# Optimization experiments

Measured on AMD Instinct MI355X. Metric: run time of the kernel, lower is better.

## Reference

```python
import jax, jax.numpy as jnp
import numpy as np

B = 32
N = 1024  # half_size == num_delays == num_wavelength
DELTA_TAU = 1.5e-15
W_CENTER = 1.175e15  # center_frequency / 2
PULSE_THRESHOLD = 0.01
PENALTY = 10.0
REAL_W = 1.0; IMAG_W = 1.0; INT_W = 1.0; PHASE_W = 1.0; FROG_W = 1.0
MSE_WSUM = REAL_W + IMAG_W + INT_W + PHASE_W

# Hilbert mask exactly as in the torch source (even N branch): H[N//2+1:]=2, H[N//2]=1
_Hm = np.zeros(N, dtype=np.float32)
_Hm[N // 2 + 1:] = 2.0
_Hm[N // 2] = 1.0
HILBERT_MASK = jnp.asarray(_Hm)

# precomputed circular-shift gather indices: shifted[m, j] = x[(j - delay[m]) mod N]
_delays = np.arange(-(N // 2), N // 2)
SHIFT_IDX = jnp.asarray((np.arange(N)[None, :] - _delays[:, None]) % N)  # [N, N] int
SHIFT_FACTOR = jnp.exp(-1j * jnp.asarray(2.0 * W_CENTER * DELTA_TAU * _delays, dtype=jnp.float32)).astype(jnp.complex64)  # [N]


def hilbert(x):  # x: [N] real -> [N] complex analytical signal
    xf = jnp.fft.fft(x)
    return jnp.fft.ifft(xf * HILBERT_MASK)


def shg_mat(a):  # a: [N] complex -> [N, N] complex SHG matrix (vectorized createSHGmat)
    shifted = a[SHIFT_IDX]                                  # [N, N] all circular shifts
    rows = a[None, :] * shifted * SHIFT_FACTOR[None, :]     # elementwise complex multiply
    f = jnp.fft.fft(jnp.fft.fftshift(rows, axes=-1), axis=-1)  # one batched FFT
    return DELTA_TAU * jnp.fft.fftshift(f, axes=-1)


def _first_last(mask):  # mask: [B, N] bool -> per-sample first/last significant index with fallback
    any_m = jnp.any(mask, axis=1)
    first = jnp.where(any_m, jnp.argmax(mask, axis=1), 0)
    last = jnp.where(any_m, N - 1 - jnp.argmax(mask[:, ::-1], axis=1), N - 1)
    return first, last


def setup_inputs() -> dict:
    key = jax.random.key(0)
    k1, k2, k3 = jax.random.split(key, 3)
    prediction = jax.random.normal(k1, (B, N), dtype=jnp.float32)
    label = jax.random.normal(k2, (B, 2 * N), dtype=jnp.float32)
    shg_matrix = jax.random.uniform(k3, (B, 1, N, N), dtype=jnp.float32)
    return {"prediction": prediction, "label": label, "shg_matrix": shg_matrix}


def reference(prediction, label, shg_matrix):
    pa = jax.vmap(hilbert)(prediction)          # [B, N] complex64
    pr, pi = pa.real, pa.imag
    lr, li = label[:, :N], label[:, N:]
    l_int = lr ** 2 + li ** 2
    p_int = pr ** 2 + pi ** 2
    l_ph = jnp.arctan2(li, lr)
    p_ph = jnp.arctan2(pi, pr)

    # ---- FROG error ----
    shg_pred = jnp.abs(jax.vmap(shg_mat)(pa)) ** 2              # [B, N, N]
    shg_pred = shg_pred / jnp.max(shg_pred, axis=(1, 2), keepdims=True)  # normalizeSHGmatrix
    t_ref = shg_matrix[:, 0]                                    # [B, N, N]
    sum1 = jnp.sum(shg_pred * t_ref, axis=(1, 2))
    sum2 = jnp.sum(t_ref * t_ref, axis=(1, 2))
    mu = sum1 / sum2
    r = jnp.sum(shg_pred - mu[:, None, None] * t_ref, axis=(1, 2)) ** 2
    norm = (N * N) * jnp.max(shg_pred, axis=(1, 2)) ** 2
    frog = jnp.where(r == 0.0, 0.0, jnp.sqrt(r / norm))         # [B]

    # ---- weighted masked MSE ----
    fr, lr_idx = _first_last(jnp.abs(lr) > PULSE_THRESHOLD)
    fi, li_idx = _first_last(jnp.abs(li) > PULSE_THRESHOLD)
    first = jnp.minimum(fr, fi)
    last = jnp.maximum(lr_idx, li_idx)
    ar = jnp.arange(N)[None, :]
    in_range = (ar >= first[:, None]) & (ar < last[:, None])    # [first:last] slice semantics
    phase_mask = in_range.astype(jnp.float32)
    pulse_mask = jnp.where(in_range, PENALTY, 1.0)

    mse_real = jnp.mean((pr - lr) ** 2 * pulse_mask, axis=1) * REAL_W
    mse_imag = jnp.mean((pi - li) ** 2 * pulse_mask, axis=1) * IMAG_W
    mse_int = jnp.mean((p_int - l_int) ** 2 * pulse_mask, axis=1) * INT_W
    mse_ph = jnp.mean((p_ph - l_ph) ** 2 * phase_mask, axis=1) * PHASE_W
    mse = (mse_real + mse_imag + mse_int + mse_ph) / MSE_WSUM

    return jnp.mean(mse + FROG_W * frog)
```

## Files before the change

### kernel.cpp

```cpp
#include <hip/hip_runtime.h>
#include <math.h>

#define N 1024
#define BATCH 32
#define NT 256
#define ROWS 4

#define WSYNC() asm volatile("s_waitcnt lgkmcnt(0)" ::: "memory")

typedef float2 cf;
__device__ __forceinline__ cf cadd(cf a, cf b){ return make_float2(a.x+b.x, a.y+b.y); }
__device__ __forceinline__ cf csub(cf a, cf b){ return make_float2(a.x-b.x, a.y-b.y); }
__device__ __forceinline__ cf cmul(cf a, cf b){ return make_float2(a.x*b.x - a.y*b.y, a.x*b.y + a.y*b.x); }

__device__ __forceinline__ cf twiddle(float jn){
    float s = __builtin_amdgcn_sinf(jn);
    float c = __builtin_amdgcn_cosf(jn);
    return make_float2(c, -s);
}

__device__ __forceinline__ void bfly(cf x0, cf x1, cf x2, cf x3,
                                     cf& y0, cf& y1, cf& y2, cf& y3){
    cf A = cadd(x0,x2), Bs = cadd(x1,x3);
    cf C = csub(x0,x2), D = csub(x1,x3);
    cf Dmi = make_float2(D.y, -D.x);
    y0 = cadd(A,Bs); y1 = cadd(C,Dmi); y2 = csub(A,Bs); y3 = csub(C,Dmi);
}

__global__ __launch_bounds__(64) void hconv_k(const float* __restrict__ pred,
                                              const float* __restrict__ label,
                                              cf* __restrict__ a,
                                              cf* __restrict__ ca,
                                              float* __restrict__ mseP) {
    __shared__ float xe[512], xo[512], C2[1024];
    int l = threadIdx.x, blk = blockIdx.x;
    int b = blk >> 3, oct = blk & 7;
    const float* xr = pred + b * N;

    float4 q0 = *(const float4*)(xr + 16 * l);
    float4 q1 = *(const float4*)(xr + 16 * l + 4);
    float4 q2 = *(const float4*)(xr + 16 * l + 8);
    float4 q3 = *(const float4*)(xr + 16 * l + 12);
    *(float4*)&xe[8 * l]     = make_float4(q0.x, q0.z, q1.x, q1.z);
    *(float4*)&xe[8 * l + 4] = make_float4(q2.x, q2.z, q3.x, q3.z);
    *(float4*)&xo[8 * l]     = make_float4(q0.y, q0.w, q1.y, q1.w);
    *(float4*)&xo[8 * l + 4] = make_float4(q2.y, q2.w, q3.y, q3.w);
    float lsum = q0.x+q0.y+q0.z+q0.w + q1.x+q1.y+q1.z+q1.w
               + q2.x+q2.y+q2.z+q2.w + q3.x+q3.y+q3.z+q3.w;
    for (int o = 32; o > 0; o >>= 1) lsum += __shfl_down(lsum, o);
    float mean = __shfl(lsum, 0) * (1.f / 1024.f);

#pragma unroll
    for (int k = 0; k < 16; ++k) {
        int u = l + 64 * k;
        int j = u & 511;
        float th = (float)(2 * j + 1) * (3.14159274f / 1024.f);
        C2[u] = -(cosf(th) / sinf(th)) * (1.f / 512.f);
    }
    WSYNC();

    int v = oct * 64 + l;
    int P = v + 512;
    float acc_e = 0.f, acc_o = 0.f;
    float c_hi = C2[P];
    for (int c = 0; c < 128; ++c) {
        float4 xep = *(const float4*)&xe[4 * c];
        float4 xop = *(const float4*)&xo[4 * c];
        float c0 = C2[P - 1 - 4 * c];
        float c1 = C2[P - 2 - 4 * c];
        float c2 = C2[P - 3 - 4 * c];
        float c3 = C2[P - 4 - 4 * c];
        acc_e += xop.x * c0;  acc_o += xep.x * c_hi;
        acc_e += xop.y * c1;  acc_o += xep.y * c0;
        acc_e += xop.z * c2;  acc_o += xep.z * c1;
        acc_e += xop.w * c3;  acc_o += xep.w * c2;
        c_hi = c3;
    }

    int ne = 2 * v, no = ne + 1;
    float axe = xe[v] - mean, axo = xo[v] - mean;
    *(float4*)&a[b * N + ne] = make_float4(axe, acc_e, axo, acc_o);
    float pe = (float)(3.525 * (double)(ne - 512));
    float po = (float)(3.525 * (double)(no - 512));
    float se, cE, so_, cO;
    sincosf(pe, &se, &cE);
    sincosf(po, &so_, &cO);
    *(float4*)&ca[b * N + ne] = make_float4(axe * cE + acc_e * se, acc_e * cE - axe * se,
                                            axo * cO + acc_o * so_, acc_o * cO - axo * so_);

    const float* lab = label + b * 2 * N;
    int mnR = N, mxR = -1, mnI = N, mxI = -1;
#pragma unroll
    for (int k = 0; k < 16; ++k) {
        int n = l + 64 * k;
        float lr = lab[n], li = lab[N + n];
        if (fabsf(lr) > 0.01f) { mnR = min(mnR, n); mxR = max(mxR, n); }
        if (fabsf(li) > 0.01f) { mnI = min(mnI, n); mxI = max(mxI, n); }
    }
    for (int o = 32; o > 0; o >>= 1) {
        mnR = min(mnR, __shfl_down(mnR, o));
        mxR = max(mxR, __shfl_down(mxR, o));
        mnI = min(mnI, __shfl_down(mnI, o));
        mxI = max(mxI, __shfl_down(mxI, o));
    }
    mnR = __shfl(mnR, 0); mxR = __shfl(mxR, 0);
    mnI = __shfl(mnI, 0); mxI = __shfl(mxI, 0);
    int fr   = (mnR == N) ? 0 : mnR;
    int lstR = (mxR < 0) ? (N - 1) : mxR;
    int fi   = (mnI == N) ? 0 : mnI;
    int lstI = (mxI < 0) ? (N - 1) : mxI;
    int first = min(fr, fi), last = max(lstR, lstI);

    float s_lane = 0.f;
    {
        float lr = lab[ne], li = lab[N + ne];
        bool in = (ne >= first) && (ne < last);
        float pm = in ? 10.f : 1.f, phm = in ? 1.f : 0.f;
        float dr = axe - lr, di = acc_e - li;
        float dn = (axe * axe + acc_e * acc_e) - (lr * lr + li * li);
        float dp = atan2f(acc_e, axe) - atan2f(li, lr);
        s_lane += (dr * dr + di * di + dn * dn) * pm + dp * dp * phm;

        lr = lab[no]; li = lab[N + no];
        in = (no >= first) && (no < last);
        pm = in ? 10.f : 1.f; phm = in ? 1.f : 0.f;
        dr = axo - lr; di = acc_o - li;
        dn = (axo * axo + acc_o * acc_o) - (lr * lr + li * li);
        dp = atan2f(acc_o, axo) - atan2f(li, lr);
        s_lane += (dr * dr + di * di + dn * dn) * pm + dp * dp * phm;
    }
    for (int o = 32; o > 0; o >>= 1) s_lane += __shfl_down(s_lane, o);
    if (l == 0) mseP[blk] = s_lane;
}

__global__ __launch_bounds__(NT) void shg_k(const cf* __restrict__ a,
                                            const cf* __restrict__ cag,
                                            const float* __restrict__ tref,
                                            float* __restrict__ Praw,
                                            float* __restrict__ Prt,
                                            float* __restrict__ Pmax,
                                            float* __restrict__ Pt,
                                            float* __restrict__ Ptt) {
    __shared__ cf wk[ROWS * N];
    int t = threadIdx.x, blk = blockIdx.x;
    int b = blk >> 8;
    int dg = (blk & 255) << 2;
    const cf* arow  = a   + b * N;
    const cf* carow = cag + b * N;

    int r3 = t >> 6;
    int g  = t & 63;
    int bd = b * N + dg + r3;
    int kb = ((g & 3) << 4) | (g & 12) | (g >> 4);
    const float* trow2 = tref + ((size_t)bd << 10) + kb;
    float tv[16];
#pragma unroll
    for (int u = 0; u < 4; ++u)
#pragma unroll
        for (int m = 0; m < 4; ++m)
            tv[4*u + m] = trow2[(((m + 2) & 3) << 8) | (u << 6)];

    {
        int bt = t;
        cf w1 = twiddle((float)bt * (1.0f / 1024.0f));
        cf w2 = cmul(w1,w1), w3 = cmul(w2,w1);
        cf cv[4];
#pragma unroll
        for (int j = 0; j < 4; ++j) cv[j] = carow[bt + 256*j];
        int wb = bt ^ (((bt >> 4) & 7) << 1);
#pragma unroll
        for (int r = 0; r < ROWS; ++r) {
            int d = dg + r;
            cf x[4];
#pragma unroll
            for (int k = 0; k < 4; ++k)
                x[k] = cmul(cv[(k + 2) & 3], arow[(bt + 256*k - d) & 1023]);
            cf y0, y1, y2, y3; bfly(x[0],x[1],x[2],x[3],y0,y1,y2,y3);
            cf* w = wk + r * N + wb;
            w[0]   = y0;
            w[256] = cmul(y1,w1);
            w[512] = cmul(y2,w2);
            w[768] = cmul(y3,w3);
        }
    }
    __syncthreads();

    __builtin_amdgcn_s_setprio(1);
    {
        int r  = t >> 6;
        int q2 = t & 63;
        int B2 = q2 >> 4;
        int v  = q2 & 15;
        cf* w = wk + r * N + B2 * 256;
        cf p[16];
#pragma unroll
        for (int m = 0; m < 16; ++m) p[m] = w[16*m + (v ^ ((m & 7) << 1))];
        {
            const cf T16 = { 0.923879533f, -0.382683432f };
            cf w1 = twiddle((float)v * (1.0f / 256.0f));
#pragma unroll
            for (int m0 = 0; m0 < 4; ++m0) {
                cf w2 = cmul(w1,w1), w3 = cmul(w2,w1);
                cf y0, y1, y2, y3;
                bfly(p[m0], p[m0+4], p[m0+8], p[m0+12], y0,y1,y2,y3);
                p[m0]    = y0;
                p[m0+4]  = cmul(y1,w1);
                p[m0+8]  = cmul(y2,w2);
                p[m0+12] = cmul(y3,w3);
                w1 = cmul(w1, T16);
            }
        }
        {
            cf w1 = twiddle((float)v * (1.0f / 64.0f));
            cf w2 = cmul(w1,w1), w3 = cmul(w2,w1);
#pragma unroll
            for (int s = 0; s < 4; ++s) {
                cf y0, y1, y2, y3;
                bfly(p[4*s], p[4*s+1], p[4*s+2], p[4*s+3], y0,y1,y2,y3);
                p[4*s]   = y0;
                p[4*s+1] = cmul(y1,w1);
                p[4*s+2] = cmul(y2,w2);
                p[4*s+3] = cmul(y3,w3);
            }
        }
#pragma unroll
        for (int m = 0; m < 16; ++m) w[16*m + (v ^ ((m & 7) << 1))] = p[m];
    }
    WSYNC();

    {
        const cf W1 = { 0.923879533f, -0.382683432f};
        const cf W2 = { 0.707106781f, -0.707106781f};
        const cf W3 = { 0.382683432f, -0.923879533f};
        const cf W6 = {-0.707106781f, -0.707106781f};
        const cf W9 = {-0.923879533f,  0.382683432f};
        cf* w = wk + r3 * N + 16 * g;
        int X = (g & 7) << 1;
        cf v[16];
#pragma unroll
        for (int j = 0; j < 8; ++j) {
            float4 q = *(const float4*)&w[(2*j) ^ X];
            v[2*j]   = make_float2(q.x, q.y);
            v[2*j+1] = make_float2(q.z, q.w);
        }
        cf o[16];
        bfly(v[0], v[4], v[8], v[12], o[0], o[4], o[8],  o[12]);
        { cf y0,y1,y2,y3; bfly(v[1],v[5],v[9], v[13],y0,y1,y2,y3);
          o[1]=y0; o[5]=cmul(y1,W1); o[9]=cmul(y2,W2); o[13]=cmul(y3,W3); }
        { cf y0,y1,y2,y3; bfly(v[2],v[6],v[10],v[14],y0,y1,y2,y3);
          o[2]=y0; o[6]=cmul(y1,W2); o[10]=make_float2(y2.y,-y2.x); o[14]=cmul(y3,W6); }
        { cf y0,y1,y2,y3; bfly(v[3],v[7],v[11],v[15],y0,y1,y2,y3);
          o[3]=y0; o[7]=cmul(y1,W3); o[11]=cmul(y2,W6); o[15]=cmul(y3,W9); }

        float sraw = 0.f, srt = 0.f, mx = 0.f, st = 0.f, stt = 0.f;
#pragma unroll
        for (int u = 0; u < 4; ++u) {
            cf y0, y1, y2, y3;
            bfly(o[4*u], o[4*u+1], o[4*u+2], o[4*u+3], y0, y1, y2, y3);
            cf ys[4] = {y0, y1, y2, y3};
#pragma unroll
            for (int m = 0; m < 4; ++m) {
                float m2 = ys[m].x * ys[m].x + ys[m].y * ys[m].y;
                float tvv = tv[4*u + m];
                sraw += m2;
                srt += m2 * tvv;
                mx = fmaxf(mx, m2);
                st += tvv;
                stt += tvv * tvv;
            }
        }
        __builtin_amdgcn_s_setprio(0);
        for (int o_ = 32; o_ > 0; o_ >>= 1) {
            sraw += __shfl_down(sraw, o_);
            srt  += __shfl_down(srt, o_);
            mx    = fmaxf(mx, __shfl_down(mx, o_));
            st   += __shfl_down(st, o_);
            stt  += __shfl_down(stt, o_);
        }
        if ((t & 63) == 0) {
            Praw[bd] = sraw; Prt[bd] = srt; Pmax[bd] = mx; Pt[bd] = st; Ptt[bd] = stt;
        }
    }
}

__global__ __launch_bounds__(256) void loss_k(const float* __restrict__ Praw,
                                              const float* __restrict__ Prt,
                                              const float* __restrict__ Pmax,
                                              const float* __restrict__ Pt,
                                              const float* __restrict__ Ptt,
                                              const float* __restrict__ mseP,
                                              float* __restrict__ out) {
    __shared__ float rbuf[4][8];
    int tid = threadIdx.x, b = blockIdx.x;
    int w = tid >> 6, lane = tid & 63;
    float sr = 0.f, srt = 0.f, mx = 0.f, st = 0.f, stt = 0.f;
    for (int i = tid; i < N; i += 256) {
        int idx = b * N + i;
        sr += Praw[idx]; srt += Prt[idx]; mx = fmaxf(mx, Pmax[idx]);
        st += Pt[idx];   stt += Ptt[idx];
    }
    for (int o = 32; o > 0; o >>= 1) {
        sr  += __shfl_down(sr, o);
        srt += __shfl_down(srt, o);
        mx   = fmaxf(mx, __shfl_down(mx, o));
        st  += __shfl_down(st, o);
        stt += __shfl_down(stt, o);
    }
    if (lane == 0) {
        rbuf[w][0] = sr; rbuf[w][1] = srt; rbuf[w][2] = mx;
        rbuf[w][3] = st; rbuf[w][4] = stt;
    }
    __syncthreads();
    if (tid == 0) {
        float A0 = 0.f, A1 = 0.f, A2 = 0.f, A3 = 0.f, A4 = 0.f;
        for (int i = 0; i < 4; ++i) {
            A0 += rbuf[i][0]; A1 += rbuf[i][1]; A2 = fmaxf(A2, rbuf[i][2]);
            A3 += rbuf[i][3]; A4 += rbuf[i][4];
        }
        float mu = (A1 / A2) / A4;
        float diff = A0 / A2 - mu * A3;
        float frog = fabsf(diff) * (1.f / (float)N);
        float ms = 0.f;
        for (int k = 0; k < 8; ++k) ms += mseP[b * 8 + k];
        ms *= (1.f / (float)N) * 0.25f;
        atomicAdd(out, (ms + frog) * (1.f / (float)BATCH));
    }
}

extern "C" void kernel_launch(void* const* d_in, const int* in_sizes, int n_in,
                              void* d_out, int out_size, void* d_ws, size_t ws_size,
                              hipStream_t stream) {
    (void)in_sizes; (void)n_in; (void)out_size; (void)ws_size;
    const float* pred  = (const float*)d_in[0];
    const float* label = (const float*)d_in[1];
    const float* shg   = (const float*)d_in[2];
    float* out = (float*)d_out;

    char* ws = (char*)d_ws;
    cf* a   = (cf*)ws;
    cf* ca  = a + (size_t)BATCH * N;
    float* mseP = (float*)(ca + (size_t)BATCH * N);
    float* P = mseP + BATCH * 8;
    float* Praw = P;
    float* Prt  = P + (size_t)BATCH * N;
    float* Pmax = P + 2 * (size_t)BATCH * N;
    float* Pt   = P + 3 * (size_t)BATCH * N;
    float* Ptt  = P + 4 * (size_t)BATCH * N;

    hipMemsetAsync(d_out, 0, sizeof(float), stream);
    hconv_k<<<BATCH * 8, 64, 0, stream>>>(pred, label, a, ca, mseP);
    shg_k<<<BATCH * 256, NT, 0, stream>>>(a, ca, shg, Praw, Prt, Pmax, Pt, Ptt);
    loss_k<<<BATCH, 256, 0, stream>>>(Praw, Prt, Pmax, Pt, Ptt, mseP, out);
}
```

Before: 228.8 us.

## Assign one wavefront per SHG row to replace block barrier with wave-local sync

The first radix-4 FFT stage is remapped so each 64-lane wavefront builds the whole row it later transforms, looping over four column groups with a rotating twiddle. Because rows are no longer shared across waves, the block-wide __syncthreads is replaced by an LDS waitcnt, so each wave can move ahead independently. The cost is more loads per thread of the shifted input and of the cag row, and each thread now steps its twiddle by repeated complex multiplication. Correctness rests on each wave only reading LDS entries it wrote itself.

```diff
diff --git a/kernel.cpp b/kernel.cpp
--- a/kernel.cpp
+++ b/kernel.cpp
@@ -150,6 +150,7 @@
 
     int r3 = t >> 6;
     int g  = t & 63;
+
     int bd = b * N + dg + r3;
     int kb = ((g & 3) << 4) | (g & 12) | (g >> 4);
     const float* trow2 = tref + ((size_t)bd << 10) + kb;
@@ -161,37 +162,38 @@
             tv[4*u + m] = trow2[(((m + 2) & 3) << 8) | (u << 6)];
 
     {
-        int bt = t;
-        cf w1 = twiddle((float)bt * (1.0f / 1024.0f));
-        cf w2 = cmul(w1,w1), w3 = cmul(w2,w1);
-        cf cv[4];
-#pragma unroll
-        for (int j = 0; j < 4; ++j) cv[j] = carow[bt + 256*j];
-        int wb = bt ^ (((bt >> 4) & 7) << 1);
-#pragma unroll
-        for (int r = 0; r < ROWS; ++r) {
-            int d = dg + r;
-            cf x[4];
-#pragma unroll
-            for (int k = 0; k < 4; ++k)
-                x[k] = cmul(cv[(k + 2) & 3], arow[(bt + 256*k - d) & 1023]);
-            cf y0, y1, y2, y3; bfly(x[0],x[1],x[2],x[3],y0,y1,y2,y3);
-            cf* w = wk + r * N + wb;
-            w[0]   = y0;
-            w[256] = cmul(y1,w1);
-            w[512] = cmul(y2,w2);
-            w[768] = cmul(y3,w3);
-        }
-    }
-    __syncthreads();
+        int d = dg + r3;
+        cf* wrow = wk + r3 * N;
+        const cf T64 = { 0.923879533f, -0.382683432f };
+        cf w1 = twiddle((float)g * (1.0f / 1024.0f));
+#pragma unroll
+        for (int s = 0; s < 4; ++s) {
+            int bt = g + 64 * s;
+            cf cv0 = carow[bt];
+            cf cv1 = carow[bt + 256];
+            cf cv2 = carow[bt + 512];
+            cf cv3 = carow[(bt + 768) & 1023];
+            cf x0 = cmul(cv2, arow[(bt       - d) & 1023]);
+            cf x1 = cmul(cv3, arow[(bt + 256 - d) & 1023]);
+            cf x2 = cmul(cv0, arow[(bt + 512 - d) & 1023]);
+            cf x3 = cmul(cv1, arow[(bt + 768 - d) & 1023]);
+            cf y0, y1, y2, y3; bfly(x0,x1,x2,x3,y0,y1,y2,y3);
+            cf w2 = cmul(w1,w1), w3 = cmul(w2,w1);
+            int wb = bt ^ (((bt >> 4) & 7) << 1);
+            wrow[wb]       = y0;
+            wrow[wb + 256] = cmul(y1,w1);
+            wrow[wb + 512] = cmul(y2,w2);
+            wrow[wb + 768] = cmul(y3,w3);
+            w1 = cmul(w1, T64);
+        }
+    }
+    WSYNC();
 
     __builtin_amdgcn_s_setprio(1);
     {
-        int r  = t >> 6;
-        int q2 = t & 63;
-        int B2 = q2 >> 4;
-        int v  = q2 & 15;
-        cf* w = wk + r * N + B2 * 256;
+        int B2 = g >> 4;
+        int v  = g & 15;
+        cf* w = wk + r3 * N + B2 * 256;
         cf p[16];
 #pragma unroll
         for (int m = 0; m < 16; ++m) p[m] = w[16*m + (v ^ ((m & 7) << 1))];
@@ -277,7 +279,7 @@
             st   += __shfl_down(st, o_);
             stt  += __shfl_down(stt, o_);
         }
-        if ((t & 63) == 0) {
+        if (g == 0) {
             Praw[bd] = sraw; Prt[bd] = srt; Pmax[bd] = mx; Pt[bd] = st; Ptt[bd] = stt;
         }
     }
```

New measurement: 242.1 us. 1.06x slower.
